# Optimization experiments

Hardware: AMD Instinct MI355X
Metric: run time of the kernel (lower is better)

The kernel has to match this reference:

```python
import jax, jax.numpy as jnp
import numpy as np

NUM_CODES = 4096
EMBED_DIM = 64
BETA = 0.25


def setup_inputs() -> dict:
    key = jax.random.key(0)
    k1, k2 = jax.random.split(key)
    z = jax.random.normal(k1, (8, EMBED_DIM, 64, 64), dtype=jnp.float32)
    weight = jax.random.normal(k2, (NUM_CODES, EMBED_DIM), dtype=jnp.float32)
    return {"z": z, "weight": weight}


def reference(z, weight):
    # z: [B, C, H, W] -> [B, H, W, C]
    z_bhwc = jnp.moveaxis(z, 1, -1)
    z_flat = z_bhwc.reshape(-1, EMBED_DIM)  # [N, d]

    # squared-euclidean distances: ||z||^2 + ||w||^2 - 2 z.w  -> [N, num_codes]
    distance = (
        jnp.sum(z_flat ** 2, axis=1, keepdims=True)
        + jnp.sum(weight ** 2, axis=1)
        - 2.0 * jnp.einsum('bd,nd->bn', z_flat, weight)
    )
    encoding_indices = jnp.argmin(distance, axis=1)  # [N]

    # codebook lookup (gather)
    z_q = weight[encoding_indices].reshape(z_bhwc.shape)  # [B, H, W, C]

    encodings = jax.nn.one_hot(encoding_indices, NUM_CODES, dtype=z.dtype)  # [N, num_codes]
    avg_probs = jnp.mean(encodings, axis=0)
    tiny = 1e-10  # max(1e-10, finfo(fp32).tiny)
    perplexity = jnp.exp(-jnp.sum(avg_probs * jnp.log(avg_probs + tiny)))

    # commitment loss (z_q detached) — eval path, no EMA state update
    loss = BETA * jnp.mean((jax.lax.stop_gradient(z_q) - z_bhwc) ** 2)

    # straight-through estimator
    z_q = z_bhwc + jax.lax.stop_gradient(z_q - z_bhwc)
    z_q = jnp.moveaxis(z_q, -1, 1)  # back to [B, C, H, W]

    return z_q, loss, perplexity, encodings, encoding_indices
```

## Files before the change

kernel.cpp:

```cpp
#include <hip/hip_runtime.h>
#include <math.h>
#include <float.h>

#define ZQ_OFF   0
#define LOSS_OFF 2097152
#define PERP_OFF 2097153
#define ENC_OFF  2097154
#define IDX_OFF  136314882ULL
#define BETA     0.25f


typedef __attribute__((ext_vector_type(8))) short short8;
typedef __attribute__((ext_vector_type(4))) float f32x4;
typedef __attribute__((ext_vector_type(2))) float f32x2;

#define MFMA16(a, b, c) __builtin_amdgcn_mfma_f32_16x16x32_bf16(a, b, c, 0, 0, 0)

__device__ __forceinline__ float bf16_rn(float v, unsigned short* h) {
    unsigned u = __float_as_uint(v);
    unsigned r = (u + 0x7fffu + ((u >> 16) & 1u)) & 0xffff0000u;
    *h = (unsigned short)(r >> 16);
    return __uint_as_float(r);
}
__device__ __forceinline__ void split3(float v, unsigned short* h, unsigned short* m, unsigned short* l) {
    float hf = bf16_rn(v, h);
    float r1 = v - hf;
    float mf = bf16_rn(r1, m);
    float r2 = r1 - mf;
    bf16_rn(r2, l);
}

__global__ void vq_wnorm(const float* __restrict__ w, float* __restrict__ wnorm) {
    int c = blockIdx.x * 256 + threadIdx.x;
    const float4* w4 = (const float4*)(w + ((size_t)c << 6));
    float s = 0.f;
    #pragma unroll
    for (int k = 0; k < 16; ++k) { float4 v = w4[k]; s += v.x*v.x + v.y*v.y + v.z*v.z + v.w*v.w; }
    wnorm[c] = s;
}

__global__ void vq_prep(const float* __restrict__ w, unsigned short* __restrict__ w3) {
    int u = blockIdx.x * 256 + threadIdx.x;
    int c = u >> 5, slot = u & 31;
    if (slot >= 24) return;
    int p = slot >> 3, g = slot & 7;
    float4 v0 = *(const float4*)(w + ((size_t)c << 6) + g * 8);
    float4 v1 = *(const float4*)(w + ((size_t)c << 6) + g * 8 + 4);
    float vv[8] = {v0.x, v0.y, v0.z, v0.w, v1.x, v1.y, v1.z, v1.w};
    short8 o;
    #pragma unroll
    for (int e = 0; e < 8; ++e) {
        unsigned short h, m, l;
        split3(vv[e], &h, &m, &l);
        o[e] = (short)((p == 0) ? h : (p == 1) ? m : l);
    }
    char* dst = (char*)w3 + (size_t)c * 384 + (((unsigned)slot * 16) ^ (((unsigned)c & 7) << 4));
    *(short8*)dst = o;
}

__global__ __launch_bounds__(256, 2) void vq_main(
    const float* __restrict__ z, const float* __restrict__ w,
    const float* __restrict__ wnorm, const unsigned short* __restrict__ w3,
    float* __restrict__ out,
    float* __restrict__ loss_ws, int* __restrict__ ticket, int* __restrict__ hist)
{
    __shared__ __align__(16) char wl[2 * 4 * 6144];
    __shared__ float snorm[4096];
    __shared__ int s_widx[64];
    __shared__ int s_flag;

    const int tx    = threadIdx.x;
    const int lane  = tx & 63;
    const int wv    = tx >> 6;
    const int rh    = wv & 1;
    const int chalf = wv >> 1;
    const int lcol  = lane & 15;
    const int lkq   = lane >> 4;
    const int base  = blockIdx.x * 64;
    const int bb    = base >> 12;
    const int hh    = (base & 4095) >> 6;

    const char* w3b = (const char*)w3;

    {
        const char* s0 = w3b + (size_t)(chalf * 16) * 384 + (size_t)lane * 16;
        char* d0 = wl + wv * 6144;
        #pragma unroll
        for (int i = 0; i < 6; ++i)
            __builtin_amdgcn_global_load_lds(
                (const __attribute__((address_space(1))) void*)(s0 + i * 1024),
                (__attribute__((address_space(3))) void*)(d0 + i * 1024), 16, 0, 0);
    }

    float (*zS)[64] = (float (*)[64])(wl + 24576);
    #pragma unroll
    for (int j = 0; j < 4; ++j) {
        int f4 = j * 256 + tx;
        int d  = f4 >> 4, w4i = f4 & 15;
        float4 v = *(const float4*)(z + (((size_t)bb * 64 + d) * 64 + hh) * 64 + w4i * 4);
        *(float4*)&zS[d][w4i * 4] = v;
    }
    #pragma unroll
    for (int j = 0; j < 4; ++j) {
        int c4 = (j * 256 + tx) * 4;
        *(float4*)&snorm[c4] = *(const float4*)(wnorm + c4);
    }
    __syncthreads();

    short8 aH[2][2], aM[2][2], aL[2][2];
    #pragma unroll
    for (int u = 0; u < 2; ++u)
        #pragma unroll
        for (int s = 0; s < 2; ++s)
            #pragma unroll
            for (int j = 0; j < 8; ++j) {
                float v = zS[s * 32 + lkq * 8 + j][rh * 32 + u * 16 + lcol];
                unsigned short h, m, l;
                split3(v, &h, &m, &l);
                aH[u][s][j] = (short)h; aM[u][s][j] = (short)m; aL[u][s][j] = (short)l;
            }
    __builtin_amdgcn_sched_barrier(0);
    __builtin_amdgcn_s_barrier();
    __builtin_amdgcn_sched_barrier(0);

    float best[2][4]; int bidx[2][4];
    #pragma unroll
    for (int u = 0; u < 2; ++u)
        #pragma unroll
        for (int r = 0; r < 4; ++r) { best[u][r] = FLT_MAX; bidx[u][r] = 0; }

    float* enc = out + ENC_OFF;
    const unsigned sw = ((unsigned)lcol & 7) << 4;
    const f32x2 zero2 = {0.f, 0.f};

    #pragma unroll 1
    for (int ch = 0; ch < 128; ++ch) {
        {
            const char* s0 = w3b + (size_t)((((ch + 1) & 127) * 32 + chalf * 16)) * 384
                           + (size_t)lane * 16;
            char* d0 = wl + ((~ch & 1) * 4 + wv) * 6144;
            #pragma unroll
            for (int i = 0; i < 6; ++i)
                __builtin_amdgcn_global_load_lds(
                    (const __attribute__((address_space(1))) void*)(s0 + i * 1024),
                    (__attribute__((address_space(3))) void*)(d0 + i * 1024), 16, 0, 0);
        }
        {
            f32x2* rowp = (f32x2*)(enc + ((size_t)(base + (ch >> 1)) << 12));
            #pragma unroll
            for (int j = 0; j < 4; ++j) {
                int slot = (ch & 1) * 1024 + ((j * 256 + tx + 7) & 1023);
                __builtin_nontemporal_store(zero2, rowp + slot);
            }
        }
        __builtin_amdgcn_sched_barrier(0);
        asm volatile("s_waitcnt vmcnt(14)" ::: "memory");
        __builtin_amdgcn_sched_barrier(0);

        {
            const int code0 = ch * 32 + chalf * 16;
            const char* rowp = wl + ((ch & 1) * 4 + wv) * 6144 + lcol * 384;
            short8 bH0 = *(const short8*)(rowp + ((lkq * 16      ) ^ sw));
            short8 bH1 = *(const short8*)(rowp + ((lkq * 16 +  64) ^ sw));
            short8 bM0 = *(const short8*)(rowp + ((lkq * 16 + 128) ^ sw));
            short8 bM1 = *(const short8*)(rowp + ((lkq * 16 + 192) ^ sw));
            short8 bL0 = *(const short8*)(rowp + ((lkq * 16 + 256) ^ sw));
            short8 bL1 = *(const short8*)(rowp + ((lkq * 16 + 320) ^ sw));
            const float wnv = snorm[code0 + lcol];
            #pragma unroll
            for (int u = 0; u < 2; ++u) {
                f32x4 c0 = {0.f,0.f,0.f,0.f}, c1 = {0.f,0.f,0.f,0.f}, c2 = {0.f,0.f,0.f,0.f};
                c0 = MFMA16(aH[u][0], bH0, c0); c0 = MFMA16(aH[u][1], bH1, c0);
                c1 = MFMA16(aH[u][0], bM0, c1); c1 = MFMA16(aH[u][1], bM1, c1);
                c1 = MFMA16(aM[u][0], bH0, c1); c1 = MFMA16(aM[u][1], bH1, c1);
                c2 = MFMA16(aM[u][0], bM0, c2); c2 = MFMA16(aM[u][1], bM1, c2);
                c2 = MFMA16(aH[u][0], bL0, c2); c2 = MFMA16(aH[u][1], bL1, c2);
                c2 = MFMA16(aL[u][0], bH0, c2); c2 = MFMA16(aL[u][1], bH1, c2);
                #pragma unroll
                for (int r = 0; r < 4; ++r) {
                    float sdot = (c0[r] + c1[r]) + c2[r];
                    float dd = fmaf(-2.f, sdot, wnv);
                    if (dd < best[u][r]) { best[u][r] = dd; bidx[u][r] = code0 + lcol; }
                }
            }
        }
    }

    __syncthreads();

    #pragma unroll
    for (int u = 0; u < 2; ++u)
        #pragma unroll
        for (int mm = 1; mm < 16; mm <<= 1)
            #pragma unroll
            for (int r = 0; r < 4; ++r) {
                float ob = __shfl_xor(best[u][r], mm, 64);
                int   oi = __shfl_xor(bidx[u][r], mm, 64);
                if (ob < best[u][r] || (ob == best[u][r] && oi < bidx[u][r])) {
                    best[u][r] = ob; bidx[u][r] = oi;
                }
            }

    float2* s_red = (float2*)snorm;
    if (lcol == 0) {
        #pragma unroll
        for (int u = 0; u < 2; ++u)
            #pragma unroll
            for (int r = 0; r < 4; ++r) {
                int row = rh * 32 + u * 16 + lkq * 4 + r;
                s_red[row * 2 + chalf] = make_float2(best[u][r], __int_as_float(bidx[u][r]));
            }
    }
    __syncthreads();

    if (tx < 64) {
        float2 a = s_red[tx * 2], b2 = s_red[tx * 2 + 1];
        int ai = __float_as_int(a.y), bi2 = __float_as_int(b2.y);
        int bi;
        if (a.x < b2.x || (a.x == b2.x && ai < bi2)) bi = ai; else bi = bi2;
        s_widx[tx] = bi;
        __builtin_nontemporal_store((float)bi, out + IDX_OFF + (size_t)(base + tx));
        atomicAdd(&hist[bi], 1);
        enc[((size_t)(base + tx) << 12) + bi] = 1.0f;
    }
    __syncthreads();

    {
        const int row = tx & 63;
        const int dg  = tx >> 6;
        const int wi  = s_widx[row];
        const float* qrow = w + ((size_t)wi << 6);
        float lsum = 0.f;
        #pragma unroll
        for (int dd = 0; dd < 16; ++dd) {
            int d = dg * 16 + dd;
            float qv = qrow[d];
            float zv = z[(((size_t)bb * 64 + d) * 64 + hh) * 64 + row];
            float diff = qv - zv;
            lsum += diff * diff;
            __builtin_nontemporal_store(zv + (qv - zv),
                out + ZQ_OFF + (((size_t)bb * 64 + d) * 64 + hh) * 64 + row);
        }
        #pragma unroll
        for (int off = 32; off > 0; off >>= 1) lsum += __shfl_down(lsum, off, 64);
        if ((tx & 63) == 0) atomicAdd(loss_ws, lsum);
    }

    __syncthreads();
    if (tx == 0) {
        __threadfence();
        int old = atomicAdd(ticket, 1);
        s_flag = (old == 511) ? 1 : 0;
    }
    __syncthreads();
    if (s_flag) {
        __threadfence();
        float s = 0.f;
        #pragma unroll
        for (int j = 0; j < 16; ++j) {
            int c = tx + j * 256;
            int cnt = atomicAdd(&hist[c], 0);
            float p = (float)cnt * (1.f / 32768.f);
            s += p * logf(p + 1e-10f);
        }
        float* fr = snorm;
        fr[tx] = s;
        __syncthreads();
        for (int off = 128; off > 0; off >>= 1) {
            if (tx < off) fr[tx] += fr[tx + off];
            __syncthreads();
        }
        if (tx == 0) {
            out[LOSS_OFF] = BETA * atomicAdd(loss_ws, 0.f) / 2097152.f;
            out[PERP_OFF] = expf(-fr[0]);
        }
    }
}

extern "C" void kernel_launch(void* const* d_in, const int* in_sizes, int n_in,
                              void* d_out, int out_size, void* d_ws, size_t ws_size,
                              hipStream_t stream)
{
    const float* z = (const float*)d_in[0];
    const float* w = (const float*)d_in[1];
    float* out     = (float*)d_out;
    float* loss_ws = (float*)d_ws;
    int*   ticket  = (int*)((char*)d_ws + 4);
    int*   hist    = (int*)((char*)d_ws + 16);
    float* wnorm   = (float*)((char*)d_ws + 16400);
    unsigned short* w3 = (unsigned short*)((char*)d_ws + 32800);
    (void)ws_size; (void)in_sizes; (void)n_in; (void)out_size;

    hipMemsetAsync(d_ws, 0, 16 + 4096 * sizeof(int), stream);
    vq_wnorm<<<16, 256, 0, stream>>>(w, wnorm);
    vq_prep<<<512, 256, 0, stream>>>(w, w3);
    vq_main<<<512, 256, 0, stream>>>(z, w, wnorm, w3, out, loss_ws, ticket, hist);
}
```

Measured before the change: 609.7 us.

## Load codebook fragments directly from global into registers instead of via LDS

Changes the prep kernel's codebook split layout so each lane's MFMA B-operand fragment is contiguous in global memory. The main loop then reads these fragments straight into registers, replacing the double-buffered global_load_lds staging and its manual waitcnt. This frees roughly 48KB of LDS, so occupancy can rise to three blocks per CU, and the loop is unrolled by two. The epilogue also reuses the z tile already in shared memory rather than reloading it from global. In exchange, global load latency is no longer explicitly prefetched and has to be hidden by the extra occupancy and unrolling.

```diff
diff --git a/kernel.cpp b/kernel.cpp
--- a/kernel.cpp
+++ b/kernel.cpp
@@ -54,17 +54,18 @@
         split3(vv[e], &h, &m, &l);
         o[e] = (short)((p == 0) ? h : (p == 1) ? m : l);
     }
-    char* dst = (char*)w3 + (size_t)c * 384 + (((unsigned)slot * 16) ^ (((unsigned)c & 7) << 4));
-    *(short8*)dst = o;
-}
-
-__global__ __launch_bounds__(256, 2) void vq_main(
+    size_t db = (size_t)((((c >> 4) * 3 + p) * 2 + (g >> 2)) * 4 + (g & 3)) * 256
+              + (size_t)(c & 15) * 16;
+    *(short8*)((char*)w3 + db) = o;
+}
+
+__global__ __launch_bounds__(256, 3) void vq_main(
     const float* __restrict__ z, const float* __restrict__ w,
     const float* __restrict__ wnorm, const unsigned short* __restrict__ w3,
     float* __restrict__ out,
     float* __restrict__ loss_ws, int* __restrict__ ticket, int* __restrict__ hist)
 {
-    __shared__ __align__(16) char wl[2 * 4 * 6144];
+    __shared__ float zS[64][64];
     __shared__ float snorm[4096];
     __shared__ int s_widx[64];
     __shared__ int s_flag;
@@ -80,19 +81,6 @@
     const int bb    = base >> 12;
     const int hh    = (base & 4095) >> 6;
 
-    const char* w3b = (const char*)w3;
-
-    {
-        const char* s0 = w3b + (size_t)(chalf * 16) * 384 + (size_t)lane * 16;
-        char* d0 = wl + wv * 6144;
-        #pragma unroll
-        for (int i = 0; i < 6; ++i)
-            __builtin_amdgcn_global_load_lds(
-                (const __attribute__((address_space(1))) void*)(s0 + i * 1024),
-                (__attribute__((address_space(3))) void*)(d0 + i * 1024), 16, 0, 0);
-    }
-
-    float (*zS)[64] = (float (*)[64])(wl + 24576);
     #pragma unroll
     for (int j = 0; j < 4; ++j) {
         int f4 = j * 256 + tx;
@@ -119,9 +107,6 @@
                 split3(v, &h, &m, &l);
                 aH[u][s][j] = (short)h; aM[u][s][j] = (short)m; aL[u][s][j] = (short)l;
             }
-    __builtin_amdgcn_sched_barrier(0);
-    __builtin_amdgcn_s_barrier();
-    __builtin_amdgcn_sched_barrier(0);
 
     float best[2][4]; int bidx[2][4];
     #pragma unroll
@@ -130,21 +115,20 @@
         for (int r = 0; r < 4; ++r) { best[u][r] = FLT_MAX; bidx[u][r] = 0; }
 
     float* enc = out + ENC_OFF;
-    const unsigned sw = ((unsigned)lcol & 7) << 4;
     const f32x2 zero2 = {0.f, 0.f};
-
-    #pragma unroll 1
+    const char* wsrc = (const char*)w3 + (size_t)lane * 16;
+
+    #pragma unroll 2
     for (int ch = 0; ch < 128; ++ch) {
-        {
-            const char* s0 = w3b + (size_t)((((ch + 1) & 127) * 32 + chalf * 16)) * 384
-                           + (size_t)lane * 16;
-            char* d0 = wl + ((~ch & 1) * 4 + wv) * 6144;
-            #pragma unroll
-            for (int i = 0; i < 6; ++i)
-                __builtin_amdgcn_global_load_lds(
-                    (const __attribute__((address_space(1))) void*)(s0 + i * 1024),
-                    (__attribute__((address_space(3))) void*)(d0 + i * 1024), 16, 0, 0);
-        }
+        const int code0 = ch * 32 + chalf * 16;
+        const char* bp = wsrc + (size_t)(ch * 2 + chalf) * 6144;
+        short8 bH0 = *(const short8*)(bp);
+        short8 bH1 = *(const short8*)(bp + 1024);
+        short8 bM0 = *(const short8*)(bp + 2048);
+        short8 bM1 = *(const short8*)(bp + 3072);
+        short8 bL0 = *(const short8*)(bp + 4096);
+        short8 bL1 = *(const short8*)(bp + 5120);
+
         {
             f32x2* rowp = (f32x2*)(enc + ((size_t)(base + (ch >> 1)) << 12));
             #pragma unroll
@@ -153,35 +137,22 @@
                 __builtin_nontemporal_store(zero2, rowp + slot);
             }
         }
-        __builtin_amdgcn_sched_barrier(0);
-        asm volatile("s_waitcnt vmcnt(14)" ::: "memory");
-        __builtin_amdgcn_sched_barrier(0);
-
-        {
-            const int code0 = ch * 32 + chalf * 16;
-            const char* rowp = wl + ((ch & 1) * 4 + wv) * 6144 + lcol * 384;
-            short8 bH0 = *(const short8*)(rowp + ((lkq * 16      ) ^ sw));
-            short8 bH1 = *(const short8*)(rowp + ((lkq * 16 +  64) ^ sw));
-            short8 bM0 = *(const short8*)(rowp + ((lkq * 16 + 128) ^ sw));
-            short8 bM1 = *(const short8*)(rowp + ((lkq * 16 + 192) ^ sw));
-            short8 bL0 = *(const short8*)(rowp + ((lkq * 16 + 256) ^ sw));
-            short8 bL1 = *(const short8*)(rowp + ((lkq * 16 + 320) ^ sw));
-            const float wnv = snorm[code0 + lcol];
-            #pragma unroll
-            for (int u = 0; u < 2; ++u) {
-                f32x4 c0 = {0.f,0.f,0.f,0.f}, c1 = {0.f,0.f,0.f,0.f}, c2 = {0.f,0.f,0.f,0.f};
-                c0 = MFMA16(aH[u][0], bH0, c0); c0 = MFMA16(aH[u][1], bH1, c0);
-                c1 = MFMA16(aH[u][0], bM0, c1); c1 = MFMA16(aH[u][1], bM1, c1);
-                c1 = MFMA16(aM[u][0], bH0, c1); c1 = MFMA16(aM[u][1], bH1, c1);
-                c2 = MFMA16(aM[u][0], bM0, c2); c2 = MFMA16(aM[u][1], bM1, c2);
-                c2 = MFMA16(aH[u][0], bL0, c2); c2 = MFMA16(aH[u][1], bL1, c2);
-                c2 = MFMA16(aL[u][0], bH0, c2); c2 = MFMA16(aL[u][1], bH1, c2);
-                #pragma unroll
-                for (int r = 0; r < 4; ++r) {
-                    float sdot = (c0[r] + c1[r]) + c2[r];
-                    float dd = fmaf(-2.f, sdot, wnv);
-                    if (dd < best[u][r]) { best[u][r] = dd; bidx[u][r] = code0 + lcol; }
-                }
+
+        const float wnv = snorm[code0 + lcol];
+        #pragma unroll
+        for (int u = 0; u < 2; ++u) {
+            f32x4 c0 = {0.f,0.f,0.f,0.f}, c1 = {0.f,0.f,0.f,0.f}, c2 = {0.f,0.f,0.f,0.f};
+            c0 = MFMA16(aH[u][0], bH0, c0); c0 = MFMA16(aH[u][1], bH1, c0);
+            c1 = MFMA16(aH[u][0], bM0, c1); c1 = MFMA16(aH[u][1], bM1, c1);
+            c1 = MFMA16(aM[u][0], bH0, c1); c1 = MFMA16(aM[u][1], bH1, c1);
+            c2 = MFMA16(aM[u][0], bM0, c2); c2 = MFMA16(aM[u][1], bM1, c2);
+            c2 = MFMA16(aH[u][0], bL0, c2); c2 = MFMA16(aH[u][1], bL1, c2);
+            c2 = MFMA16(aL[u][0], bH0, c2); c2 = MFMA16(aL[u][1], bH1, c2);
+            #pragma unroll
+            for (int r = 0; r < 4; ++r) {
+                float sdot = (c0[r] + c1[r]) + c2[r];
+                float dd = fmaf(-2.f, sdot, wnv);
+                if (dd < best[u][r]) { best[u][r] = dd; bidx[u][r] = code0 + lcol; }
             }
         }
     }
@@ -235,7 +206,7 @@
         for (int dd = 0; dd < 16; ++dd) {
             int d = dg * 16 + dd;
             float qv = qrow[d];
-            float zv = z[(((size_t)bb * 64 + d) * 64 + hh) * 64 + row];
+            float zv = zS[d][row];
             float diff = qv - zv;
             lsum += diff * diff;
             __builtin_nontemporal_store(zv + (qv - zv),
```

New measurement: 663.4 us. +8.8%, slower.

## Share codebook tiles across waves in LDS and raise occupancy to three blocks

Applied to the files above, without the earlier changes.

The codebook split layout is reorganized into 16-code tiles in MFMA fragment order, so each lane reads contiguous 16-byte chunks without XOR swizzling. Each chunk of 32 codes is now loaded cooperatively by all four waves into a shared 12 KB buffer, instead of each wave pair loading duplicate copies. This halves LDS footprint and global-to-LDS traffic, allowing three blocks per CU. In exchange it adds two workgroup barriers per iteration, and the z staging now runs before the first codebook prefetch.

```diff
diff --git a/kernel.cpp b/kernel.cpp
--- a/kernel.cpp
+++ b/kernel.cpp
@@ -54,17 +54,18 @@
         split3(vv[e], &h, &m, &l);
         o[e] = (short)((p == 0) ? h : (p == 1) ? m : l);
     }
-    char* dst = (char*)w3 + (size_t)c * 384 + (((unsigned)slot * 16) ^ (((unsigned)c & 7) << 4));
-    *(short8*)dst = o;
-}
-
-__global__ __launch_bounds__(256, 2) void vq_main(
+    size_t db = (size_t)((((c >> 4) * 3 + p) * 2 + (g >> 2)) * 4 + (g & 3)) * 256
+              + (size_t)(c & 15) * 16;
+    *(short8*)((char*)w3 + db) = o;
+}
+
+__global__ __launch_bounds__(256, 3) void vq_main(
     const float* __restrict__ z, const float* __restrict__ w,
     const float* __restrict__ wnorm, const unsigned short* __restrict__ w3,
     float* __restrict__ out,
     float* __restrict__ loss_ws, int* __restrict__ ticket, int* __restrict__ hist)
 {
-    __shared__ __align__(16) char wl[2 * 4 * 6144];
+    __shared__ __align__(16) char wl[2 * 12288];
     __shared__ float snorm[4096];
     __shared__ int s_widx[64];
     __shared__ int s_flag;
@@ -82,17 +83,7 @@
 
     const char* w3b = (const char*)w3;
 
-    {
-        const char* s0 = w3b + (size_t)(chalf * 16) * 384 + (size_t)lane * 16;
-        char* d0 = wl + wv * 6144;
-        #pragma unroll
-        for (int i = 0; i < 6; ++i)
-            __builtin_amdgcn_global_load_lds(
-                (const __attribute__((address_space(1))) void*)(s0 + i * 1024),
-                (__attribute__((address_space(3))) void*)(d0 + i * 1024), 16, 0, 0);
-    }
-
-    float (*zS)[64] = (float (*)[64])(wl + 24576);
+    float (*zS)[64] = (float (*)[64])wl;
     #pragma unroll
     for (int j = 0; j < 4; ++j) {
         int f4 = j * 256 + tx;
@@ -123,6 +114,20 @@
     __builtin_amdgcn_s_barrier();
     __builtin_amdgcn_sched_barrier(0);
 
+    {
+        const char* s0 = w3b + wv * 3072 + (size_t)lane * 16;
+        char* d0 = wl + wv * 3072;
+        #pragma unroll
+        for (int i = 0; i < 3; ++i)
+            __builtin_amdgcn_global_load_lds(
+                (const __attribute__((address_space(1))) void*)(s0 + i * 1024),
+                (__attribute__((address_space(3))) void*)(d0 + i * 1024), 16, 0, 0);
+    }
+    __builtin_amdgcn_sched_barrier(0);
+    asm volatile("s_waitcnt vmcnt(0)" ::: "memory");
+    __builtin_amdgcn_s_barrier();
+    __builtin_amdgcn_sched_barrier(0);
+
     float best[2][4]; int bidx[2][4];
     #pragma unroll
     for (int u = 0; u < 2; ++u)
@@ -130,21 +135,23 @@
         for (int r = 0; r < 4; ++r) { best[u][r] = FLT_MAX; bidx[u][r] = 0; }
 
     float* enc = out + ENC_OFF;
-    const unsigned sw = ((unsigned)lcol & 7) << 4;
     const f32x2 zero2 = {0.f, 0.f};
 
     #pragma unroll 1
     for (int ch = 0; ch < 128; ++ch) {
+        char* nxt = wl + (~ch & 1) * 12288;
+
         {
-            const char* s0 = w3b + (size_t)((((ch + 1) & 127) * 32 + chalf * 16)) * 384
+            const char* s0 = w3b + (size_t)((ch + 1) & 127) * 12288 + wv * 3072
                            + (size_t)lane * 16;
-            char* d0 = wl + ((~ch & 1) * 4 + wv) * 6144;
-            #pragma unroll
-            for (int i = 0; i < 6; ++i)
+            char* d0 = nxt + wv * 3072;
+            #pragma unroll
+            for (int i = 0; i < 3; ++i)
                 __builtin_amdgcn_global_load_lds(
                     (const __attribute__((address_space(1))) void*)(s0 + i * 1024),
                     (__attribute__((address_space(3))) void*)(d0 + i * 1024), 16, 0, 0);
         }
+        __builtin_amdgcn_sched_barrier(0);
         {
             f32x2* rowp = (f32x2*)(enc + ((size_t)(base + (ch >> 1)) << 12));
             #pragma unroll
@@ -154,18 +161,19 @@
             }
         }
         __builtin_amdgcn_sched_barrier(0);
-        asm volatile("s_waitcnt vmcnt(14)" ::: "memory");
+        asm volatile("s_waitcnt vmcnt(11)" ::: "memory");
+        __builtin_amdgcn_s_barrier();
         __builtin_amdgcn_sched_barrier(0);
 
         {
             const int code0 = ch * 32 + chalf * 16;
-            const char* rowp = wl + ((ch & 1) * 4 + wv) * 6144 + lcol * 384;
-            short8 bH0 = *(const short8*)(rowp + ((lkq * 16      ) ^ sw));
-            short8 bH1 = *(const short8*)(rowp + ((lkq * 16 +  64) ^ sw));
-            short8 bM0 = *(const short8*)(rowp + ((lkq * 16 + 128) ^ sw));
-            short8 bM1 = *(const short8*)(rowp + ((lkq * 16 + 192) ^ sw));
-            short8 bL0 = *(const short8*)(rowp + ((lkq * 16 + 256) ^ sw));
-            short8 bL1 = *(const short8*)(rowp + ((lkq * 16 + 320) ^ sw));
+            const char* bufc = wl + (ch & 1) * 12288 + chalf * 6144 + (size_t)lane * 16;
+            short8 bH0 = *(const short8*)(bufc);
+            short8 bH1 = *(const short8*)(bufc + 1024);
+            short8 bM0 = *(const short8*)(bufc + 2048);
+            short8 bM1 = *(const short8*)(bufc + 3072);
+            short8 bL0 = *(const short8*)(bufc + 4096);
+            short8 bL1 = *(const short8*)(bufc + 5120);
             const float wnv = snorm[code0 + lcol];
             #pragma unroll
             for (int u = 0; u < 2; ++u) {
@@ -184,6 +192,8 @@
                 }
             }
         }
+        __builtin_amdgcn_sched_barrier(0);
+        __builtin_amdgcn_s_barrier();
     }
 
     __syncthreads();
```

Result: slower. 623.8 us (+2.3%).
